# Kernel tuning notes

Hardware: AMD Instinct MI355X
Metric: run time of the kernel (lower is better)

## Reference

```python
import jax, jax.numpy as jnp
import numpy as np

B, T, HORIZON = 64, 12, 12
N, E, K, H = 1024, 8, 3, 64
DIN, DOUT, YCOV = 1, 1, 1


def setup_inputs() -> dict:
    key = jax.random.key(0)
    ks = jax.random.split(key, 8)

    def xavier(k, shape):
        std = (2.0 / (shape[0] + shape[1])) ** 0.5
        return jax.random.normal(k, shape, jnp.float32) * std

    return {
        "x": jax.random.normal(ks[0], (B, T, N, DIN), jnp.float32),
        "y_cov": jax.random.normal(ks[1], (B, HORIZON, N, YCOV), jnp.float32),
        "node_embeddings": jax.random.normal(ks[2], (N, E), jnp.float32),
        "enc_gate_W": xavier(ks[3], (K * (DIN + H), 2 * H)),
        "enc_gate_b": jnp.zeros((2 * H,), jnp.float32),
        "enc_upd_W": xavier(ks[4], (K * (DIN + H), H)),
        "enc_upd_b": jnp.zeros((H,), jnp.float32),
        "dec_gate_W": xavier(ks[5], (K * (DOUT + YCOV + H), 2 * H)),
        "dec_gate_b": jnp.zeros((2 * H,), jnp.float32),
        "dec_upd_W": xavier(ks[6], (K * (DOUT + YCOV + H), H)),
        "dec_upd_b": jnp.zeros((H,), jnp.float32),
        "proj_W": xavier(ks[7], (H, DOUT)),
        "proj_b": jnp.zeros((DOUT,), jnp.float32),
    }


def _cheb(support, k):
    # Chebyshev polynomial set: T0=I, T1=A, Tk = 2*A@T_{k-1} - T_{k-2}
    mats = [jnp.eye(support.shape[0], dtype=support.dtype), support]
    for _ in range(2, k):
        mats.append(2.0 * (support @ mats[-1]) - mats[-2])
    return jnp.stack(mats)  # [K, N, N]


def _gcn(x, supports, W, b):
    # x: [B,N,C]; supports: [K,N,N] -> gather [B,N,K,C], concat k-major as in torch.cat
    xg = jnp.einsum('knm,bmc->bnkc', supports, x)
    Bb, Nn, Kk, Cc = xg.shape
    return xg.reshape(Bb, Nn, Kk * Cc) @ W + b


def _cell(x, state, supports, gW, gb, uW, ub):
    zr = jax.nn.sigmoid(_gcn(jnp.concatenate([x, state], axis=-1), supports, gW, gb))
    z, r = jnp.split(zr, 2, axis=-1)
    hc = jnp.tanh(_gcn(jnp.concatenate([x, z * state], axis=-1), supports, uW, ub))
    return r * state + (1.0 - r) * hc


def reference(x, y_cov, node_embeddings, enc_gate_W, enc_gate_b, enc_upd_W,
              enc_upd_b, dec_gate_W, dec_gate_b, dec_upd_W, dec_upd_b,
              proj_W, proj_b):
    # adaptive adjacency: softmax(relu(E E^T), axis=1)
    support = jax.nn.softmax(jax.nn.relu(node_embeddings @ node_embeddings.T), axis=1)
    supports = _cheb(support, K)

    # encoder over T_in steps (single rnn layer)
    h0 = jnp.zeros((x.shape[0], N, H), x.dtype)

    def enc_step(h, xt):
        h = _cell(xt, h, supports, enc_gate_W, enc_gate_b, enc_upd_W, enc_upd_b)
        return h, None

    h_t, _ = jax.lax.scan(enc_step, h0, jnp.swapaxes(x, 0, 1))

    go0 = jnp.zeros((x.shape[0], N, DOUT), x.dtype)

    def dec_step(carry, yt):
        go, h = carry
        h = _cell(jnp.concatenate([go, yt], axis=-1), h, supports,
                  dec_gate_W, dec_gate_b, dec_upd_W, dec_upd_b)
        go = h @ proj_W + proj_b
        return (go, h), go

    _, outs = jax.lax.scan(dec_step, (go0, h_t), jnp.swapaxes(y_cov, 0, 1))
    return jnp.swapaxes(outs, 0, 1)  # [B, horizon, N, output_dim]
```

## Files before the change

### kernel.cpp

```cpp
#include <hip/hip_runtime.h>


typedef __attribute__((ext_vector_type(8))) short bf16x8;
typedef __attribute__((ext_vector_type(4))) float f32x4;
typedef __attribute__((ext_vector_type(4))) unsigned short u16x4;

__device__ __forceinline__ float b2f(unsigned short u) {
    union { unsigned int i; float f; } v; v.i = ((unsigned int)u) << 16; return v.f;
}
__device__ __forceinline__ unsigned short f2b(float f) {
    union { float f; unsigned int i; } v; v.f = f;
    unsigned int r = v.i + 0x7FFFu + ((v.i >> 16) & 1u);
    return (unsigned short)(r >> 16);
}

#define GLOAD_LDS16(g, l) __builtin_amdgcn_global_load_lds( \
    (const __attribute__((address_space(1))) void*)(g),     \
    (__attribute__((address_space(3))) void*)(l), 16, 0, 0)

__global__ __launch_bounds__(256) void gemm_bt(
    const unsigned short* __restrict__ P, int lda,
    const unsigned short* __restrict__ QT, int ldb,
    unsigned short* __restrict__ C, int ldc,
    int K, float scale)
{
    __shared__ __align__(16) unsigned short As[128 * 32];
    __shared__ __align__(16) unsigned short Bs[128 * 32];
    const int tid = threadIdx.x;
    const int m0 = blockIdx.y << 7, n0 = blockIdx.x << 7;
    const int w = tid >> 6, l = tid & 63;
    const int wm = (w >> 1) << 6, wn = (w & 1) << 6;
    const int lr = l & 15, lq = l >> 4;
    const int arow = tid >> 2, ak = (tid & 3) << 3;
    f32x4 acc[4][4] = {};

    for (int k0 = 0; k0 < K; k0 += 32) {
#pragma unroll
        for (int p = 0; p < 2; ++p)
            GLOAD_LDS16(P + (size_t)(m0 + arow + (p << 6)) * lda + k0 + ak,
                        &As[((arow + (p << 6)) << 5) + ak]);
#pragma unroll
        for (int p = 0; p < 2; ++p)
            GLOAD_LDS16(QT + (size_t)(n0 + arow + (p << 6)) * ldb + k0 + ak,
                        &Bs[((arow + (p << 6)) << 5) + ak]);
        __syncthreads();
        bf16x8 a[4], b[4];
#pragma unroll
        for (int i = 0; i < 4; ++i)
            a[i] = *(const bf16x8*)&As[((wm + (i << 4) + lr) << 5) + (lq << 3)];
#pragma unroll
        for (int j = 0; j < 4; ++j)
            b[j] = *(const bf16x8*)&Bs[((wn + (j << 4) + lr) << 5) + (lq << 3)];
#pragma unroll
        for (int i = 0; i < 4; ++i)
#pragma unroll
            for (int j = 0; j < 4; ++j)
                acc[i][j] = __builtin_amdgcn_mfma_f32_16x16x32_bf16(a[i], b[j], acc[i][j], 0, 0, 0);
        __syncthreads();
    }
#pragma unroll
    for (int i = 0; i < 4; ++i)
#pragma unroll
        for (int j = 0; j < 4; ++j)
#pragma unroll
            for (int r = 0; r < 4; ++r) {
                const int m = m0 + wm + (i << 4) + (lq << 2) + r;
                const int n = n0 + wn + (j << 4) + lr;
                C[(size_t)m * ldc + n] = f2b(acc[i][j][r] * scale);
            }
}

__global__ __launch_bounds__(256) void gru_gate(
    const unsigned short* __restrict__ Hb, const unsigned short* __restrict__ S, int ldS,
    const unsigned short* __restrict__ WT, const float* __restrict__ bias,
    const float* __restrict__ wx, const float* __restrict__ xin, int t,
    const unsigned short* __restrict__ XSgT, int xsrow, const unsigned short* __restrict__ Go,
    const float* __restrict__ H32,
    unsigned short* __restrict__ Zb, unsigned short* __restrict__ ZhT, float* __restrict__ R,
    int dec)
{
    __shared__ __align__(16) unsigned short As[128 * 32];
    __shared__ __align__(16) unsigned short Bs[128 * 32];
    const int tid = threadIdx.x;
    const int rb = blockIdx.x;
    const int b = rb >> 3, n0 = (rb & 7) << 7;
    const int w = tid >> 6, l = tid & 63;
    const int wm = (w >> 1) << 6, wn = (w & 1) << 6;
    const int lr = l & 15, lq = l >> 4;
    const int arow = tid >> 2, ak = (tid & 3) << 3;
    f32x4 acc[4][4] = {};

    const unsigned short* sbase[3];
    size_t sstride[3];
    sbase[0] = Hb + ((size_t)(b << 10) + n0) * 64;        sstride[0] = 64;
    sbase[1] = S + (size_t)n0 * ldS + (b << 6);           sstride[1] = (size_t)ldS;
    sbase[2] = S + (size_t)(1024 + n0) * ldS + (b << 6);  sstride[2] = (size_t)ldS;

    for (int kk0 = 0; kk0 < 192; kk0 += 32) {
        const int seg = kk0 >> 6, so = kk0 & 63;
#pragma unroll
        for (int p = 0; p < 2; ++p)
            GLOAD_LDS16(sbase[seg] + (size_t)(arow + (p << 6)) * sstride[seg] + so + ak,
                        &As[((arow + (p << 6)) << 5) + ak]);
#pragma unroll
        for (int p = 0; p < 2; ++p)
            GLOAD_LDS16(WT + (size_t)(arow + (p << 6)) * 192 + kk0 + ak,
                        &Bs[((arow + (p << 6)) << 5) + ak]);
        __syncthreads();
        bf16x8 a[4], bb[4];
#pragma unroll
        for (int i = 0; i < 4; ++i)
            a[i] = *(const bf16x8*)&As[((wm + (i << 4) + lr) << 5) + (lq << 3)];
#pragma unroll
        for (int j = 0; j < 4; ++j)
            bb[j] = *(const bf16x8*)&Bs[((wn + (j << 4) + lr) << 5) + (lq << 3)];
#pragma unroll
        for (int i = 0; i < 4; ++i)
#pragma unroll
            for (int j = 0; j < 4; ++j)
                acc[i][j] = __builtin_amdgcn_mfma_f32_16x16x32_bf16(a[i], bb[j], acc[i][j], 0, 0, 0);
        __syncthreads();
    }

#pragma unroll
    for (int i = 0; i < 4; ++i) {
        const int node_base = n0 + wm + (i << 4) + (lq << 2);
        float c0[4], c1[4], c2[4], c3[4], c4[4], c5[4];
        for (int r = 0; r < 4; ++r) {
            const int node = node_base + r;
            if (!dec) {
                c0[r] = xin[((b * 12 + t) << 10) + node];
                c1[r] = b2f(XSgT[(size_t)(xsrow + t * 64 + b) * 2048 + node]);
                c2[r] = b2f(XSgT[(size_t)(xsrow + t * 64 + b) * 2048 + 1024 + node]);
                c3[r] = c4[r] = c5[r] = 0.f;
            } else {
                c0[r] = b2f(Go[(b << 10) + node]);
                c1[r] = xin[((b * 12 + t) << 10) + node];
                c2[r] = b2f(S[(size_t)node * ldS + 4096 + b]);
                c3[r] = b2f(XSgT[(size_t)(xsrow + t * 64 + b) * 2048 + node]);
                c4[r] = b2f(S[(size_t)(1024 + node) * ldS + 4096 + b]);
                c5[r] = b2f(XSgT[(size_t)(xsrow + t * 64 + b) * 2048 + 1024 + node]);
            }
        }
#pragma unroll
        for (int j = 0; j < 4; ++j) {
            const int jc = wn + (j << 4) + lr;
            const float bj = bias[jc];
            const float w0 = wx[jc], w1 = wx[128 + jc], w2 = wx[256 + jc];
            float w3 = 0.f, w4 = 0.f, w5 = 0.f;
            if (dec) { w3 = wx[384 + jc]; w4 = wx[512 + jc]; w5 = wx[640 + jc]; }
            if (jc < 64) {
                u16x4 pack;
                for (int r = 0; r < 4; ++r) {
                    float v = acc[i][j][r] + bj + c0[r] * w0 + c1[r] * w1 + c2[r] * w2
                              + c3[r] * w3 + c4[r] * w4 + c5[r] * w5;
                    float g = 1.f / (1.f + __expf(-v));
                    const int node = node_base + r;
                    const size_t idx = ((size_t)(b << 10) + node) * 64 + jc;
                    float zh = g * H32[idx];
                    unsigned short zb = f2b(zh);
                    Zb[idx] = zb;
                    pack[r] = zb;
                }
                *(u16x4*)&ZhT[(size_t)((b << 6) + jc) * 1024 + node_base] = pack;
            } else {
                for (int r = 0; r < 4; ++r) {
                    float v = acc[i][j][r] + bj + c0[r] * w0 + c1[r] * w1 + c2[r] * w2
                              + c3[r] * w3 + c4[r] * w4 + c5[r] * w5;
                    float g = 1.f / (1.f + __expf(-v));
                    const int node = node_base + r;
                    R[((size_t)(b << 10) + node) * 64 + (jc - 64)] = g;
                }
            }
        }
    }
}

__global__ __launch_bounds__(256) void gru_update(
    const unsigned short* __restrict__ Zb, const unsigned short* __restrict__ S, int ldS,
    const unsigned short* __restrict__ WT, const float* __restrict__ bias,
    const float* __restrict__ wx, const float* __restrict__ xin, int t,
    const unsigned short* __restrict__ XSgT, int xsrow, const unsigned short* __restrict__ Go,
    const float* __restrict__ Rg,
    float* __restrict__ H32, unsigned short* __restrict__ Hb, unsigned short* __restrict__ XhT,
    const float* __restrict__ prW, const float* __restrict__ prb,
    unsigned short* __restrict__ GoOut, float* __restrict__ outp,
    int dec)
{
    __shared__ __align__(16) unsigned short As[128 * 32];
    __shared__ __align__(16) unsigned short Bs[64 * 32];
    const int tid = threadIdx.x;
    const int rb = blockIdx.x;
    const int b = rb >> 3, n0 = (rb & 7) << 7;
    const int w = tid >> 6, l = tid & 63;
    const int wm = w << 5;
    const int lr = l & 15, lq = l >> 4;
    const int arow = tid >> 2, ak = (tid & 3) << 3;
    f32x4 acc[2][4] = {};

    const unsigned short* sbase[3];
    size_t sstride[3];
    sbase[0] = Zb + ((size_t)(b << 10) + n0) * 64;        sstride[0] = 64;
    sbase[1] = S + (size_t)n0 * ldS + (b << 6);           sstride[1] = (size_t)ldS;
    sbase[2] = S + (size_t)(1024 + n0) * ldS + (b << 6);  sstride[2] = (size_t)ldS;

    for (int kk0 = 0; kk0 < 192; kk0 += 32) {
        const int seg = kk0 >> 6, so = kk0 & 63;
#pragma unroll
        for (int p = 0; p < 2; ++p)
            GLOAD_LDS16(sbase[seg] + (size_t)(arow + (p << 6)) * sstride[seg] + so + ak,
                        &As[((arow + (p << 6)) << 5) + ak]);
        GLOAD_LDS16(WT + (size_t)arow * 192 + kk0 + ak, &Bs[(arow << 5) + ak]);
        __syncthreads();
        bf16x8 a[2], bb[4];
#pragma unroll
        for (int i = 0; i < 2; ++i)
            a[i] = *(const bf16x8*)&As[((wm + (i << 4) + lr) << 5) + (lq << 3)];
#pragma unroll
        for (int j = 0; j < 4; ++j)
            bb[j] = *(const bf16x8*)&Bs[(((j << 4) + lr) << 5) + (lq << 3)];
#pragma unroll
        for (int i = 0; i < 2; ++i)
#pragma unroll
            for (int j = 0; j < 4; ++j)
                acc[i][j] = __builtin_amdgcn_mfma_f32_16x16x32_bf16(a[i], bb[j], acc[i][j], 0, 0, 0);
        __syncthreads();
    }

    float pw[4];
    if (dec) {
#pragma unroll
        for (int j = 0; j < 4; ++j) pw[j] = prW[(j << 4) + lr];
    }

#pragma unroll
    for (int i = 0; i < 2; ++i) {
        const int node_base = n0 + wm + (i << 4) + (lq << 2);
        float c0[4], c1[4], c2[4], c3[4], c4[4], c5[4];
        for (int r = 0; r < 4; ++r) {
            const int node = node_base + r;
            if (!dec) {
                c0[r] = xin[((b * 12 + t) << 10) + node];
                c1[r] = b2f(XSgT[(size_t)(xsrow + t * 64 + b) * 2048 + node]);
                c2[r] = b2f(XSgT[(size_t)(xsrow + t * 64 + b) * 2048 + 1024 + node]);
                c3[r] = c4[r] = c5[r] = 0.f;
            } else {
                c0[r] = b2f(Go[(b << 10) + node]);
                c1[r] = xin[((b * 12 + t) << 10) + node];
                c2[r] = b2f(S[(size_t)node * ldS + 4096 + b]);
                c3[r] = b2f(XSgT[(size_t)(xsrow + t * 64 + b) * 2048 + node]);
                c4[r] = b2f(S[(size_t)(1024 + node) * ldS + 4096 + b]);
                c5[r] = b2f(XSgT[(size_t)(xsrow + t * 64 + b) * 2048 + 1024 + node]);
            }
        }
        float psum[4] = {0.f, 0.f, 0.f, 0.f};
#pragma unroll
        for (int j = 0; j < 4; ++j) {
            const int jc = (j << 4) + lr;
            const float bj = bias[jc];
            const float w0 = wx[jc], w1 = wx[64 + jc], w2 = wx[128 + jc];
            float w3 = 0.f, w4 = 0.f, w5 = 0.f;
            if (dec) { w3 = wx[192 + jc]; w4 = wx[256 + jc]; w5 = wx[320 + jc]; }
            u16x4 pack;
            for (int r = 0; r < 4; ++r) {
                float v = acc[i][j][r] + bj + c0[r] * w0 + c1[r] * w1 + c2[r] * w2
                          + c3[r] * w3 + c4[r] * w4 + c5[r] * w5;
                float hc = tanhf(v);
                const int node = node_base + r;
                const size_t idx = ((size_t)(b << 10) + node) * 64 + jc;
                float rr = Rg[idx];
                float hn = rr * H32[idx] + (1.f - rr) * hc;
                H32[idx] = hn;
                unsigned short hb = f2b(hn);
                Hb[idx] = hb;
                pack[r] = hb;
                if (dec) psum[r] += hn * pw[j];
            }
            *(u16x4*)&XhT[(size_t)((b << 6) + jc) * 1024 + node_base] = pack;
        }
        if (dec) {
#pragma unroll
            for (int r = 0; r < 4; ++r) {
                float v = psum[r];
                v += __shfl_down(v, 8, 16);
                v += __shfl_down(v, 4, 16);
                v += __shfl_down(v, 2, 16);
                v += __shfl_down(v, 1, 16);
                if (lr == 0) {
                    const int node = node_base + r;
                    const float go = v + prb[0];
                    GoOut[(b << 10) + node] = f2b(go);
                    XhT[((size_t)(4096 + b) << 10) + node] = f2b(go);
                    outp[((size_t)(b * 12 + t) << 10) + node] = go;
                }
            }
        }
    }
}

__global__ __launch_bounds__(256) void adj_softmax(
    const float* __restrict__ E, unsigned short* __restrict__ A)
{
    __shared__ float Es[8192];
    __shared__ float vals[1024];
    __shared__ float red[8];
    const int tid = threadIdx.x;
    const int r = blockIdx.x;
    for (int i = tid; i < 8192; i += 256) Es[i] = E[i];
    __syncthreads();
    float er[8];
#pragma unroll
    for (int e = 0; e < 8; ++e) er[e] = Es[(r << 3) + e];
    float lmax = -1e30f;
    for (int c = tid; c < 1024; c += 256) {
        float s = 0.f;
#pragma unroll
        for (int e = 0; e < 8; ++e) s += er[e] * Es[(c << 3) + e];
        s = fmaxf(s, 0.f);
        vals[c] = s;
        lmax = fmaxf(lmax, s);
    }
    for (int off = 32; off; off >>= 1) lmax = fmaxf(lmax, __shfl_down(lmax, off, 64));
    if ((tid & 63) == 0) red[tid >> 6] = lmax;
    __syncthreads();
    const float m = fmaxf(fmaxf(red[0], red[1]), fmaxf(red[2], red[3]));
    float lsum = 0.f;
    for (int c = tid; c < 1024; c += 256) {
        float e = __expf(vals[c] - m);
        vals[c] = e;
        lsum += e;
    }
    for (int off = 32; off; off >>= 1) lsum += __shfl_down(lsum, off, 64);
    if ((tid & 63) == 0) red[4 + (tid >> 6)] = lsum;
    __syncthreads();
    const float inv = 1.f / (red[4] + red[5] + red[6] + red[7]);
    for (int c = tid; c < 1024; c += 256)
        A[(r << 10) + c] = f2b(vals[c] * inv);
}

__global__ __launch_bounds__(256) void transpose_bf16(
    const unsigned short* __restrict__ src, unsigned short* __restrict__ dst)
{
    __shared__ unsigned short tile[64][65];
    const int bx = blockIdx.x & 15, by = blockIdx.x >> 4;
    const int x0 = bx << 6, y0 = by << 6;
    for (int i = threadIdx.x; i < 4096; i += 256) {
        const int r = i >> 6, c = i & 63;
        tile[r][c] = src[((y0 + r) << 10) + x0 + c];
    }
    __syncthreads();
    for (int i = threadIdx.x; i < 4096; i += 256) {
        const int r = i >> 6, c = i & 63;
        dst[((x0 + r) << 10) + y0 + c] = tile[c][r];
    }
}

__global__ __launch_bounds__(256) void build_xall(
    const float* __restrict__ x, const float* __restrict__ y,
    unsigned short* __restrict__ XallT)
{
    const int id = blockIdx.x * 256 + threadIdx.x;
    const int row = id >> 10, n = id & 1023;
    int t, b;
    const float* src;
    if (row < 768) { t = row >> 6; b = row & 63; src = x; }
    else { const int rr = row - 768; t = rr >> 6; b = rr & 63; src = y; }
    XallT[id] = f2b(src[((b * 12 + t) << 10) + n]);
}

__global__ __launch_bounds__(256) void wprep(
    const float* egW, const float* egb,
    const float* euW, const float* eub,
    const float* dgW, const float* dgb,
    const float* duW, const float* dub,
    const float* pW, const float* pb,
    unsigned short* WgTe, unsigned short* WuTe, unsigned short* WgTd, unsigned short* WuTd,
    float* wxge, float* wxue, float* wxgd, float* wxud,
    float* bge, float* bue, float* bgd, float* bud,
    float* projW, float* projb)
{
    const int tid0 = blockIdx.x * 256 + threadIdx.x;
    const int stride = 256 * gridDim.x;
    for (int i = tid0; i < 128 * 192; i += stride) {
        const int j = i / 192, kk = i % 192, k = kk >> 6, c = kk & 63;
        float v = egW[(k * 65 + 1 + c) * 128 + j];
        if (k == 0) v -= egW[(131 + c) * 128 + j];
        WgTe[i] = f2b(v);
    }
    for (int i = tid0; i < 64 * 192; i += stride) {
        const int j = i / 192, kk = i % 192, k = kk >> 6, c = kk & 63;
        float v = euW[(k * 65 + 1 + c) * 64 + j];
        if (k == 0) v -= euW[(131 + c) * 64 + j];
        WuTe[i] = f2b(v);
    }
    for (int i = tid0; i < 128 * 192; i += stride) {
        const int j = i / 192, kk = i % 192, k = kk >> 6, c = kk & 63;
        float v = dgW[(k * 66 + 2 + c) * 128 + j];
        if (k == 0) v -= dgW[(134 + c) * 128 + j];
        WgTd[i] = f2b(v);
    }
    for (int i = tid0; i < 64 * 192; i += stride) {
        const int j = i / 192, kk = i % 192, k = kk >> 6, c = kk & 63;
        float v = duW[(k * 66 + 2 + c) * 64 + j];
        if (k == 0) v -= duW[(134 + c) * 64 + j];
        WuTd[i] = f2b(v);
    }
    for (int i = tid0; i < 384; i += stride) {
        const int k = i >> 7, j = i & 127;
        float v;
        if (k == 0) v = egW[j] - egW[130 * 128 + j];
        else if (k == 1) v = egW[65 * 128 + j];
        else v = egW[130 * 128 + j];
        wxge[i] = v;
    }
    for (int i = tid0; i < 192; i += stride) {
        const int k = i >> 6, j = i & 63;
        float v;
        if (k == 0) v = euW[j] - euW[130 * 64 + j];
        else if (k == 1) v = euW[65 * 64 + j];
        else v = euW[130 * 64 + j];
        wxue[i] = v;
    }
    for (int i = tid0; i < 768; i += stride) {
        const int k = i >> 7, j = i & 127;
        float v;
        switch (k) {
            case 0: v = dgW[j] - dgW[132 * 128 + j]; break;
            case 1: v = dgW[128 + j] - dgW[133 * 128 + j]; break;
            case 2: v = dgW[66 * 128 + j]; break;
            case 3: v = dgW[67 * 128 + j]; break;
            case 4: v = dgW[132 * 128 + j]; break;
            default: v = dgW[133 * 128 + j]; break;
        }
        wxgd[i] = v;
    }
    for (int i = tid0; i < 384; i += stride) {
        const int k = i >> 6, j = i & 63;
        float v;
        switch (k) {
            case 0: v = duW[j] - duW[132 * 64 + j]; break;
            case 1: v = duW[64 + j] - duW[133 * 64 + j]; break;
            case 2: v = duW[66 * 64 + j]; break;
            case 3: v = duW[67 * 64 + j]; break;
            case 4: v = duW[132 * 64 + j]; break;
            default: v = duW[133 * 64 + j]; break;
        }
        wxud[i] = v;
    }
    for (int i = tid0; i < 128; i += stride) bge[i] = egb[i];
    for (int i = tid0; i < 64; i += stride) bue[i] = eub[i];
    for (int i = tid0; i < 128; i += stride) bgd[i] = dgb[i];
    for (int i = tid0; i < 64; i += stride) bud[i] = dub[i];
    for (int i = tid0; i < 64; i += stride) projW[i] = pW[i];
    if (tid0 == 0) projb[0] = pb[0];
}

extern "C" void kernel_launch(void* const* d_in, const int* in_sizes, int n_in,
                              void* d_out, int out_size, void* d_ws, size_t ws_size,
                              hipStream_t stream)
{
    (void)in_sizes; (void)n_in; (void)out_size; (void)ws_size;
    const float* x    = (const float*)d_in[0];
    const float* ycov = (const float*)d_in[1];
    const float* E    = (const float*)d_in[2];
    const float* egW  = (const float*)d_in[3];
    const float* egb  = (const float*)d_in[4];
    const float* euW  = (const float*)d_in[5];
    const float* eub  = (const float*)d_in[6];
    const float* dgW  = (const float*)d_in[7];
    const float* dgb  = (const float*)d_in[8];
    const float* duW  = (const float*)d_in[9];
    const float* dub  = (const float*)d_in[10];
    const float* pW   = (const float*)d_in[11];
    const float* pb   = (const float*)d_in[12];
    float* out = (float*)d_out;

    size_t off = 0;
    auto carve = [&](size_t bytes) -> void* {
        void* p = (char*)d_ws + off;
        off += (bytes + 255) & ~(size_t)255;
        return p;
    };
    unsigned short* AA    = (unsigned short*)carve(2048ull * 1024 * 2);
    unsigned short* XSgT  = (unsigned short*)carve(1536ull * 2048 * 2);
    unsigned short* XhT   = (unsigned short*)carve(4224ull * 1024 * 2);
    unsigned short* ZhT   = (unsigned short*)carve(4096ull * 1024 * 2);
    unsigned short* S     = (unsigned short*)carve(2048ull * 4224 * 2);
    unsigned short* Hb    = (unsigned short*)carve(65536ull * 64 * 2);
    float*          H32   = (float*)carve(65536ull * 64 * 4);
    unsigned short* Zb    = (unsigned short*)carve(65536ull * 64 * 2);
    float*          R     = (float*)carve(65536ull * 64 * 4);
    unsigned short* Go    = (unsigned short*)carve(65536ull * 2);
    unsigned short* WgTe  = (unsigned short*)carve(128ull * 192 * 2);
    unsigned short* WuTe  = (unsigned short*)carve(64ull * 192 * 2);
    unsigned short* WgTd  = (unsigned short*)carve(128ull * 192 * 2);
    unsigned short* WuTd  = (unsigned short*)carve(64ull * 192 * 2);
    float* wxge = (float*)carve(384 * 4);
    float* wxue = (float*)carve(192 * 4);
    float* wxgd = (float*)carve(768 * 4);
    float* wxud = (float*)carve(384 * 4);
    float* bge  = (float*)carve(128 * 4);
    float* bue  = (float*)carve(64 * 4);
    float* bgd  = (float*)carve(128 * 4);
    float* bud  = (float*)carve(64 * 4);
    float* prW  = (float*)carve(64 * 4);
    float* prb  = (float*)carve(4);
    unsigned short* AT    = Zb;
    unsigned short* XallT = Zb + 1024ull * 1024;

    hipMemsetAsync(XhT, 0, 4224ull * 1024 * 2, stream);
    hipMemsetAsync(Hb, 0, 65536ull * 64 * 2, stream);
    hipMemsetAsync(H32, 0, 65536ull * 64 * 4, stream);
    hipMemsetAsync(Go, 0, 65536ull * 2, stream);

    adj_softmax<<<1024, 256, 0, stream>>>(E, AA);
    transpose_bf16<<<256, 256, 0, stream>>>(AA, AT);
    gemm_bt<<<dim3(8, 8), 256, 0, stream>>>(AA, 1024, AT, 1024, AA + 1024 * 1024, 1024, 1024, 2.0f);
    build_xall<<<6144, 256, 0, stream>>>(x, ycov, XallT);
    gemm_bt<<<dim3(16, 12), 256, 0, stream>>>(XallT, 1024, AA, 1024, XSgT, 2048, 1024, 1.0f);
    wprep<<<64, 256, 0, stream>>>(egW, egb, euW, eub, dgW, dgb, duW, dub, pW, pb,
                                  WgTe, WuTe, WgTd, WuTd, wxge, wxue, wxgd, wxud,
                                  bge, bue, bgd, bud, prW, prb);

    for (int t = 0; t < 12; ++t) {
        gemm_bt<<<dim3(32, 16), 256, 0, stream>>>(AA, 1024, XhT, 1024, S, 4224, 1024, 1.0f);
        gru_gate<<<512, 256, 0, stream>>>(Hb, S, 4224, WgTe, bge, wxge, x, t, XSgT, 0, Go, H32,
                                          Zb, ZhT, R, 0);
        gemm_bt<<<dim3(32, 16), 256, 0, stream>>>(AA, 1024, ZhT, 1024, S, 4224, 1024, 1.0f);
        gru_update<<<512, 256, 0, stream>>>(Zb, S, 4224, WuTe, bue, wxue, x, t, XSgT, 0, Go,
                                            R, H32, Hb, XhT, prW, prb, Go, out, 0);
    }
    for (int t = 0; t < 12; ++t) {
        gemm_bt<<<dim3(33, 16), 256, 0, stream>>>(AA, 1024, XhT, 1024, S, 4224, 1024, 1.0f);
        gru_gate<<<512, 256, 0, stream>>>(Hb, S, 4224, WgTd, bgd, wxgd, ycov, t, XSgT, 768, Go, H32,
                                          Zb, ZhT, R, 1);
        gemm_bt<<<dim3(32, 16), 256, 0, stream>>>(AA, 1024, ZhT, 1024, S, 4224, 1024, 1.0f);
        gru_update<<<512, 256, 0, stream>>>(Zb, S, 4224, WuTd, bud, wxud, ycov, t, XSgT, 768, Go,
                                            R, H32, Hb, XhT, prW, prb, Go, out, 1);
    }
}
```

Baseline: 2.737 ms.

## Fuse graph-support GEMM into GRU gate and update kernels via LDS

Each GRU cell stage now computes the support-times-state product (AA @ XhT or AA @ ZhT) for its own 128-node, one-batch tile inside the same kernel. The result is kept in shared memory and fed directly into the weight GEMM, so the separate gemm_bt launch and the round trip of S through global memory go away. The projected GO term is now derived algebraically from the support-times-state accumulator and prW rather than carried as an extra XhT row, with goflag zeroing it at the first decoder step. In exchange, LDS use per block grows (about 54 KB) and the 1024-long K loop runs with only 512 blocks, which may lower occupancy and parallelism.

```diff
diff --git a/kernel.cpp b/kernel.cpp
--- a/kernel.cpp
+++ b/kernel.cpp
@@ -70,61 +70,133 @@
             }
 }
 
-__global__ __launch_bounds__(256) void gru_gate(
-    const unsigned short* __restrict__ Hb, const unsigned short* __restrict__ S, int ldS,
-    const unsigned short* __restrict__ WT, const float* __restrict__ bias,
-    const float* __restrict__ wx, const float* __restrict__ xin, int t,
-    const unsigned short* __restrict__ XSgT, int xsrow, const unsigned short* __restrict__ Go,
-    const float* __restrict__ H32,
-    unsigned short* __restrict__ Zb, unsigned short* __restrict__ ZhT, float* __restrict__ R,
-    int dec)
-{
-    __shared__ __align__(16) unsigned short As[128 * 32];
+__global__ __launch_bounds__(256) void cell_gate(
+    const unsigned short* __restrict__ AA, const unsigned short* __restrict__ XhT,
+    const unsigned short* __restrict__ Hb, const unsigned short* __restrict__ WT,
+    const float* __restrict__ bias, const float* __restrict__ wx,
+    const float* __restrict__ xin, int t,
+    const unsigned short* __restrict__ XSgT, int xsrow,
+    const unsigned short* __restrict__ Go, const float* __restrict__ H32,
+    const float* __restrict__ prW, const float* __restrict__ prb,
+    float* __restrict__ Sgo,
+    unsigned short* __restrict__ Zb, unsigned short* __restrict__ ZhT,
+    float* __restrict__ R, int dec, int goflag)
+{
+    __shared__ __align__(16) unsigned short As[256 * 32];
     __shared__ __align__(16) unsigned short Bs[128 * 32];
+    __shared__ __align__(16) unsigned short Shs[256 * 72];
+    __shared__ float SgoS[256];
     const int tid = threadIdx.x;
-    const int rb = blockIdx.x;
-    const int b = rb >> 3, n0 = (rb & 7) << 7;
+    const int b = blockIdx.x >> 3, n0 = (blockIdx.x & 7) << 7;
     const int w = tid >> 6, l = tid & 63;
-    const int wm = (w >> 1) << 6, wn = (w & 1) << 6;
     const int lr = l & 15, lq = l >> 4;
     const int arow = tid >> 2, ak = (tid & 3) << 3;
-    f32x4 acc[4][4] = {};
-
-    const unsigned short* sbase[3];
-    size_t sstride[3];
-    sbase[0] = Hb + ((size_t)(b << 10) + n0) * 64;        sstride[0] = 64;
-    sbase[1] = S + (size_t)n0 * ldS + (b << 6);           sstride[1] = (size_t)ldS;
-    sbase[2] = S + (size_t)(1024 + n0) * ldS + (b << 6);  sstride[2] = (size_t)ldS;
-
+
+    {
+        const int wm = w << 6;
+        f32x4 acc[4][4] = {};
+        for (int k0 = 0; k0 < 1024; k0 += 32) {
+#pragma unroll
+            for (int p = 0; p < 4; ++p) {
+                const int row = arow + (p << 6);
+                const int grow = (p < 2) ? (n0 + row) : (896 + n0 + row);
+                GLOAD_LDS16(AA + (size_t)grow * 1024 + k0 + ak, &As[(row << 5) + ak]);
+            }
+            GLOAD_LDS16(XhT + (size_t)((b << 6) + arow) * 1024 + k0 + ak,
+                        &Bs[(arow << 5) + ak]);
+            __syncthreads();
+            bf16x8 a[4], bb[4];
+#pragma unroll
+            for (int i = 0; i < 4; ++i)
+                a[i] = *(const bf16x8*)&As[((wm + (i << 4) + lr) << 5) + (lq << 3)];
+#pragma unroll
+            for (int j = 0; j < 4; ++j)
+                bb[j] = *(const bf16x8*)&Bs[(((j << 4) + lr) << 5) + (lq << 3)];
+#pragma unroll
+            for (int i = 0; i < 4; ++i)
+#pragma unroll
+                for (int j = 0; j < 4; ++j)
+                    acc[i][j] = __builtin_amdgcn_mfma_f32_16x16x32_bf16(a[i], bb[j], acc[i][j], 0, 0, 0);
+            __syncthreads();
+        }
+#pragma unroll
+        for (int i = 0; i < 4; ++i)
+#pragma unroll
+            for (int j = 0; j < 4; ++j)
+#pragma unroll
+                for (int r = 0; r < 4; ++r) {
+                    const int m = wm + (i << 4) + (lq << 2) + r;
+                    const int c = (j << 4) + lr;
+                    Shs[m * 72 + c] = f2b(acc[i][j][r]);
+                }
+        if (dec) {
+            float pw[4];
+#pragma unroll
+            for (int j = 0; j < 4; ++j) pw[j] = prW[(j << 4) + lr];
+            const float pb0 = prb[0];
+#pragma unroll
+            for (int i = 0; i < 4; ++i)
+#pragma unroll
+                for (int r = 0; r < 4; ++r) {
+                    float v = acc[i][0][r] * pw[0] + acc[i][1][r] * pw[1]
+                            + acc[i][2][r] * pw[2] + acc[i][3][r] * pw[3];
+                    v += __shfl_down(v, 8, 16);
+                    v += __shfl_down(v, 4, 16);
+                    v += __shfl_down(v, 2, 16);
+                    v += __shfl_down(v, 1, 16);
+                    if (lr == 0) {
+                        const int m = wm + (i << 4) + (lq << 2) + r;
+                        const int grow = (m < 128) ? (n0 + m) : (896 + n0 + m);
+                        const float val = goflag
+                            ? (v + pb0 * ((m < 128) ? 1.f : 2.f)) : 0.f;
+                        Sgo[(size_t)grow * 64 + b] = val;
+                        SgoS[m] = val;
+                    }
+                }
+        }
+    }
+
+    const int wm2 = (w >> 1) << 6, wn2 = (w & 1) << 6;
+    f32x4 acc2[4][4] = {};
     for (int kk0 = 0; kk0 < 192; kk0 += 32) {
-        const int seg = kk0 >> 6, so = kk0 & 63;
-#pragma unroll
-        for (int p = 0; p < 2; ++p)
-            GLOAD_LDS16(sbase[seg] + (size_t)(arow + (p << 6)) * sstride[seg] + so + ak,
-                        &As[((arow + (p << 6)) << 5) + ak]);
 #pragma unroll
         for (int p = 0; p < 2; ++p)
             GLOAD_LDS16(WT + (size_t)(arow + (p << 6)) * 192 + kk0 + ak,
                         &Bs[((arow + (p << 6)) << 5) + ak]);
+        if (kk0 < 64) {
+#pragma unroll
+            for (int p = 0; p < 2; ++p)
+                GLOAD_LDS16(Hb + ((size_t)(b << 10) + n0 + arow + (p << 6)) * 64 + kk0 + ak,
+                            &As[((arow + (p << 6)) << 5) + ak]);
+        }
         __syncthreads();
         bf16x8 a[4], bb[4];
+        if (kk0 < 64) {
+#pragma unroll
+            for (int i = 0; i < 4; ++i)
+                a[i] = *(const bf16x8*)&As[((wm2 + (i << 4) + lr) << 5) + (lq << 3)];
+        } else {
+            const int rowb = (kk0 >= 128) ? 128 : 0;
+            const int c0 = kk0 & 63;
+#pragma unroll
+            for (int i = 0; i < 4; ++i)
+                a[i] = *(const bf16x8*)&Shs[(rowb + wm2 + (i << 4) + lr) * 72 + c0 + (lq << 3)];
+        }
+#pragma unroll
+        for (int j = 0; j < 4; ++j)
+            bb[j] = *(const bf16x8*)&Bs[((wn2 + (j << 4) + lr) << 5) + (lq << 3)];
 #pragma unroll
         for (int i = 0; i < 4; ++i)
-            a[i] = *(const bf16x8*)&As[((wm + (i << 4) + lr) << 5) + (lq << 3)];
-#pragma unroll
-        for (int j = 0; j < 4; ++j)
-            bb[j] = *(const bf16x8*)&Bs[((wn + (j << 4) + lr) << 5) + (lq << 3)];
-#pragma unroll
-        for (int i = 0; i < 4; ++i)
 #pragma unroll
             for (int j = 0; j < 4; ++j)
-                acc[i][j] = __builtin_amdgcn_mfma_f32_16x16x32_bf16(a[i], bb[j], acc[i][j], 0, 0, 0);
+                acc2[i][j] = __builtin_amdgcn_mfma_f32_16x16x32_bf16(a[i], bb[j], acc2[i][j], 0, 0, 0);
         __syncthreads();
     }
 
 #pragma unroll
     for (int i = 0; i < 4; ++i) {
-        const int node_base = n0 + wm + (i << 4) + (lq << 2);
+        const int nb_loc = wm2 + (i << 4) + (lq << 2);
+        const int node_base = n0 + nb_loc;
         float c0[4], c1[4], c2[4], c3[4], c4[4], c5[4];
         for (int r = 0; r < 4; ++r) {
             const int node = node_base + r;
@@ -136,15 +208,15 @@
             } else {
                 c0[r] = b2f(Go[(b << 10) + node]);
                 c1[r] = xin[((b * 12 + t) << 10) + node];
-                c2[r] = b2f(S[(size_t)node * ldS + 4096 + b]);
+                c2[r] = SgoS[nb_loc + r];
                 c3[r] = b2f(XSgT[(size_t)(xsrow + t * 64 + b) * 2048 + node]);
-                c4[r] = b2f(S[(size_t)(1024 + node) * ldS + 4096 + b]);
+                c4[r] = SgoS[128 + nb_loc + r];
                 c5[r] = b2f(XSgT[(size_t)(xsrow + t * 64 + b) * 2048 + 1024 + node]);
             }
         }
 #pragma unroll
         for (int j = 0; j < 4; ++j) {
-            const int jc = wn + (j << 4) + lr;
+            const int jc = wn2 + (j << 4) + lr;
             const float bj = bias[jc];
             const float w0 = wx[jc], w1 = wx[128 + jc], w2 = wx[256 + jc];
             float w3 = 0.f, w4 = 0.f, w5 = 0.f;
@@ -152,7 +224,7 @@
             if (jc < 64) {
                 u16x4 pack;
                 for (int r = 0; r < 4; ++r) {
-                    float v = acc[i][j][r] + bj + c0[r] * w0 + c1[r] * w1 + c2[r] * w2
+                    float v = acc2[i][j][r] + bj + c0[r] * w0 + c1[r] * w1 + c2[r] * w2
                               + c3[r] * w3 + c4[r] * w4 + c5[r] * w5;
                     float g = 1.f / (1.f + __expf(-v));
                     const int node = node_base + r;
@@ -165,7 +237,7 @@
                 *(u16x4*)&ZhT[(size_t)((b << 6) + jc) * 1024 + node_base] = pack;
             } else {
                 for (int r = 0; r < 4; ++r) {
-                    float v = acc[i][j][r] + bj + c0[r] * w0 + c1[r] * w1 + c2[r] * w2
+                    float v = acc2[i][j][r] + bj + c0[r] * w0 + c1[r] * w1 + c2[r] * w2
                               + c3[r] * w3 + c4[r] * w4 + c5[r] * w5;
                     float g = 1.f / (1.f + __expf(-v));
                     const int node = node_base + r;
@@ -176,46 +248,89 @@
     }
 }
 
-__global__ __launch_bounds__(256) void gru_update(
-    const unsigned short* __restrict__ Zb, const unsigned short* __restrict__ S, int ldS,
-    const unsigned short* __restrict__ WT, const float* __restrict__ bias,
-    const float* __restrict__ wx, const float* __restrict__ xin, int t,
-    const unsigned short* __restrict__ XSgT, int xsrow, const unsigned short* __restrict__ Go,
-    const float* __restrict__ Rg,
-    float* __restrict__ H32, unsigned short* __restrict__ Hb, unsigned short* __restrict__ XhT,
+__global__ __launch_bounds__(256) void cell_update(
+    const unsigned short* __restrict__ AA, const unsigned short* __restrict__ ZhT,
+    const unsigned short* __restrict__ Zb, const unsigned short* __restrict__ WT,
+    const float* __restrict__ bias, const float* __restrict__ wx,
+    const float* __restrict__ xin, int t,
+    const unsigned short* __restrict__ XSgT, int xsrow,
+    const float* __restrict__ Sgo, const float* __restrict__ Rg,
+    float* __restrict__ H32, unsigned short* __restrict__ Hb,
+    unsigned short* __restrict__ XhT,
     const float* __restrict__ prW, const float* __restrict__ prb,
-    unsigned short* __restrict__ GoOut, float* __restrict__ outp,
-    int dec)
-{
-    __shared__ __align__(16) unsigned short As[128 * 32];
+    unsigned short* __restrict__ Go, float* __restrict__ outp, int dec)
+{
+    __shared__ __align__(16) unsigned short As[256 * 32];
     __shared__ __align__(16) unsigned short Bs[64 * 32];
+    __shared__ __align__(16) unsigned short Shs[256 * 72];
     const int tid = threadIdx.x;
-    const int rb = blockIdx.x;
-    const int b = rb >> 3, n0 = (rb & 7) << 7;
+    const int b = blockIdx.x >> 3, n0 = (blockIdx.x & 7) << 7;
     const int w = tid >> 6, l = tid & 63;
-    const int wm = w << 5;
     const int lr = l & 15, lq = l >> 4;
     const int arow = tid >> 2, ak = (tid & 3) << 3;
-    f32x4 acc[2][4] = {};
-
-    const unsigned short* sbase[3];
-    size_t sstride[3];
-    sbase[0] = Zb + ((size_t)(b << 10) + n0) * 64;        sstride[0] = 64;
-    sbase[1] = S + (size_t)n0 * ldS + (b << 6);           sstride[1] = (size_t)ldS;
-    sbase[2] = S + (size_t)(1024 + n0) * ldS + (b << 6);  sstride[2] = (size_t)ldS;
-
+
+    {
+        const int wm = w << 6;
+        f32x4 acc[4][4] = {};
+        for (int k0 = 0; k0 < 1024; k0 += 32) {
+#pragma unroll
+            for (int p = 0; p < 4; ++p) {
+                const int row = arow + (p << 6);
+                const int grow = (p < 2) ? (n0 + row) : (896 + n0 + row);
+                GLOAD_LDS16(AA + (size_t)grow * 1024 + k0 + ak, &As[(row << 5) + ak]);
+            }
+            GLOAD_LDS16(ZhT + (size_t)((b << 6) + arow) * 1024 + k0 + ak,
+                        &Bs[(arow << 5) + ak]);
+            __syncthreads();
+            bf16x8 a[4], bb[4];
+#pragma unroll
+            for (int i = 0; i < 4; ++i)
+                a[i] = *(const bf16x8*)&As[((wm + (i << 4) + lr) << 5) + (lq << 3)];
+#pragma unroll
+            for (int j = 0; j < 4; ++j)
+                bb[j] = *(const bf16x8*)&Bs[(((j << 4) + lr) << 5) + (lq << 3)];
+#pragma unroll
+            for (int i = 0; i < 4; ++i)
+#pragma unroll
+                for (int j = 0; j < 4; ++j)
+                    acc[i][j] = __builtin_amdgcn_mfma_f32_16x16x32_bf16(a[i], bb[j], acc[i][j], 0, 0, 0);
+            __syncthreads();
+        }
+#pragma unroll
+        for (int i = 0; i < 4; ++i)
+#pragma unroll
+            for (int j = 0; j < 4; ++j)
+#pragma unroll
+                for (int r = 0; r < 4; ++r) {
+                    const int m = wm + (i << 4) + (lq << 2) + r;
+                    const int c = (j << 4) + lr;
+                    Shs[m * 72 + c] = f2b(acc[i][j][r]);
+                }
+    }
+
+    const int wm2 = w << 5;
+    f32x4 acc2[2][4] = {};
     for (int kk0 = 0; kk0 < 192; kk0 += 32) {
-        const int seg = kk0 >> 6, so = kk0 & 63;
-#pragma unroll
-        for (int p = 0; p < 2; ++p)
-            GLOAD_LDS16(sbase[seg] + (size_t)(arow + (p << 6)) * sstride[seg] + so + ak,
-                        &As[((arow + (p << 6)) << 5) + ak]);
         GLOAD_LDS16(WT + (size_t)arow * 192 + kk0 + ak, &Bs[(arow << 5) + ak]);
+        if (kk0 < 64) {
+#pragma unroll
+            for (int p = 0; p < 2; ++p)
+                GLOAD_LDS16(Zb + ((size_t)(b << 10) + n0 + arow + (p << 6)) * 64 + kk0 + ak,
+                            &As[((arow + (p << 6)) << 5) + ak]);
+        }
         __syncthreads();
         bf16x8 a[2], bb[4];
-#pragma unroll
-        for (int i = 0; i < 2; ++i)
-            a[i] = *(const bf16x8*)&As[((wm + (i << 4) + lr) << 5) + (lq << 3)];
+        if (kk0 < 64) {
+#pragma unroll
+            for (int i = 0; i < 2; ++i)
+                a[i] = *(const bf16x8*)&As[((wm2 + (i << 4) + lr) << 5) + (lq << 3)];
+        } else {
+            const int rowb = (kk0 >= 128) ? 128 : 0;
+            const int c0 = kk0 & 63;
+#pragma unroll
+            for (int i = 0; i < 2; ++i)
+                a[i] = *(const bf16x8*)&Shs[(rowb + wm2 + (i << 4) + lr) * 72 + c0 + (lq << 3)];
+        }
 #pragma unroll
         for (int j = 0; j < 4; ++j)
             bb[j] = *(const bf16x8*)&Bs[(((j << 4) + lr) << 5) + (lq << 3)];
@@ -223,7 +338,7 @@
         for (int i = 0; i < 2; ++i)
 #pragma unroll
             for (int j = 0; j < 4; ++j)
-                acc[i][j] = __builtin_amdgcn_mfma_f32_16x16x32_bf16(a[i], bb[j], acc[i][j], 0, 0, 0);
+                acc2[i][j] = __builtin_amdgcn_mfma_f32_16x16x32_bf16(a[i], bb[j], acc2[i][j], 0, 0, 0);
         __syncthreads();
     }
 
@@ -235,7 +350,7 @@
 
 #pragma unroll
     for (int i = 0; i < 2; ++i) {
-        const int node_base = n0 + wm + (i << 4) + (lq << 2);
+        const int node_base = n0 + wm2 + (i << 4) + (lq << 2);
         float c0[4], c1[4], c2[4], c3[4], c4[4], c5[4];
         for (int r = 0; r < 4; ++r) {
             const int node = node_base + r;
@@ -247,9 +362,9 @@
             } else {
                 c0[r] = b2f(Go[(b << 10) + node]);
                 c1[r] = xin[((b * 12 + t) << 10) + node];
-                c2[r] = b2f(S[(size_t)node * ldS + 4096 + b]);
+                c2[r] = Sgo[(size_t)node * 64 + b];
                 c3[r] = b2f(XSgT[(size_t)(xsrow + t * 64 + b) * 2048 + node]);
-                c4[r] = b2f(S[(size_t)(1024 + node) * ldS + 4096 + b]);
+                c4[r] = Sgo[(size_t)(1024 + node) * 64 + b];
                 c5[r] = b2f(XSgT[(size_t)(xsrow + t * 64 + b) * 2048 + 1024 + node]);
             }
         }
@@ -263,7 +378,7 @@
             if (dec) { w3 = wx[192 + jc]; w4 = wx[256 + jc]; w5 = wx[320 + jc]; }
             u16x4 pack;
             for (int r = 0; r < 4; ++r) {
-                float v = acc[i][j][r] + bj + c0[r] * w0 + c1[r] * w1 + c2[r] * w2
+                float v = acc2[i][j][r] + bj + c0[r] * w0 + c1[r] * w1 + c2[r] * w2
                           + c3[r] * w3 + c4[r] * w4 + c5[r] * w5;
                 float hc = tanhf(v);
                 const int node = node_base + r;
@@ -289,8 +404,7 @@
                 if (lr == 0) {
                     const int node = node_base + r;
                     const float go = v + prb[0];
-                    GoOut[(b << 10) + node] = f2b(go);
-                    XhT[((size_t)(4096 + b) << 10) + node] = f2b(go);
+                    Go[(b << 10) + node] = f2b(go);
                     outp[((size_t)(b * 12 + t) << 10) + node] = go;
                 }
             }
@@ -483,13 +597,13 @@
     };
     unsigned short* AA    = (unsigned short*)carve(2048ull * 1024 * 2);
     unsigned short* XSgT  = (unsigned short*)carve(1536ull * 2048 * 2);
-    unsigned short* XhT   = (unsigned short*)carve(4224ull * 1024 * 2);
+    unsigned short* XhT   = (unsigned short*)carve(4096ull * 1024 * 2);
     unsigned short* ZhT   = (unsigned short*)carve(4096ull * 1024 * 2);
-    unsigned short* S     = (unsigned short*)carve(2048ull * 4224 * 2);
     unsigned short* Hb    = (unsigned short*)carve(65536ull * 64 * 2);
     float*          H32   = (float*)carve(65536ull * 64 * 4);
     unsigned short* Zb    = (unsigned short*)carve(65536ull * 64 * 2);
     float*          R     = (float*)carve(65536ull * 64 * 4);
+    float*          Sgo   = (float*)carve(2048ull * 64 * 4);
     unsigned short* Go    = (unsigned short*)carve(65536ull * 2);
     unsigned short* WgTe  = (unsigned short*)carve(128ull * 192 * 2);
     unsigned short* WuTe  = (unsigned short*)carve(64ull * 192 * 2);
@@ -508,7 +622,7 @@
     unsigned short* AT    = Zb;
     unsigned short* XallT = Zb + 1024ull * 1024;
 
-    hipMemsetAsync(XhT, 0, 4224ull * 1024 * 2, stream);
+    hipMemsetAsync(XhT, 0, 4096ull * 1024 * 2, stream);
     hipMemsetAsync(Hb, 0, 65536ull * 64 * 2, stream);
     hipMemsetAsync(H32, 0, 65536ull * 64 * 4, stream);
     hipMemsetAsync(Go, 0, 65536ull * 2, stream);
@@ -523,19 +637,15 @@
                                   bge, bue, bgd, bud, prW, prb);
 
     for (int t = 0; t < 12; ++t) {
-        gemm_bt<<<dim3(32, 16), 256, 0, stream>>>(AA, 1024, XhT, 1024, S, 4224, 1024, 1.0f);
-        gru_gate<<<512, 256, 0, stream>>>(Hb, S, 4224, WgTe, bge, wxge, x, t, XSgT, 0, Go, H32,
-                                          Zb, ZhT, R, 0);
-        gemm_bt<<<dim3(32, 16), 256, 0, stream>>>(AA, 1024, ZhT, 1024, S, 4224, 1024, 1.0f);
-        gru_update<<<512, 256, 0, stream>>>(Zb, S, 4224, WuTe, bue, wxue, x, t, XSgT, 0, Go,
-                                            R, H32, Hb, XhT, prW, prb, Go, out, 0);
+        cell_gate<<<512, 256, 0, stream>>>(AA, XhT, Hb, WgTe, bge, wxge, x, t, XSgT, 0,
+                                           Go, H32, prW, prb, Sgo, Zb, ZhT, R, 0, 0);
+        cell_update<<<512, 256, 0, stream>>>(AA, ZhT, Zb, WuTe, bue, wxue, x, t, XSgT, 0,
+                                             Sgo, R, H32, Hb, XhT, prW, prb, Go, out, 0);
     }
     for (int t = 0; t < 12; ++t) {
-        gemm_bt<<<dim3(33, 16), 256, 0, stream>>>(AA, 1024, XhT, 1024, S, 4224, 1024, 1.0f);
-        gru_gate<<<512, 256, 0, stream>>>(Hb, S, 4224, WgTd, bgd, wxgd, ycov, t, XSgT, 768, Go, H32,
-                                          Zb, ZhT, R, 1);
-        gemm_bt<<<dim3(32, 16), 256, 0, stream>>>(AA, 1024, ZhT, 1024, S, 4224, 1024, 1.0f);
-        gru_update<<<512, 256, 0, stream>>>(Zb, S, 4224, WuTd, bud, wxud, ycov, t, XSgT, 768, Go,
-                                            R, H32, Hb, XhT, prW, prb, Go, out, 1);
-    }
-}
+        cell_gate<<<512, 256, 0, stream>>>(AA, XhT, Hb, WgTd, bgd, wxgd, ycov, t, XSgT, 768,
+                                           Go, H32, prW, prb, Sgo, Zb, ZhT, R, 1, t > 0 ? 1 : 0);
+        cell_update<<<512, 256, 0, stream>>>(AA, ZhT, Zb, WuTd, bud, wxud, ycov, t, XSgT, 768,
+                                             Sgo, R, H32, Hb, XhT, prW, prb, Go, out, 1);
+    }
+}
```

New measurement: 2.455 ms. 1.11x faster.
